# Kernel optimization log

Hardware: AMD Instinct MI355X
Metric: run time of the kernel (lower is better)

The kernel has to match this reference:

```python
import jax, jax.numpy as jnp
import numpy as np
import math

N = 50000
E = 800000
C_IN = 32
C_H = 256
C_OUT = 3
DEPTH = 3
RATIO = 0.5


def setup_inputs() -> dict:
    key = jax.random.key(0)
    ks = jax.random.split(key, 16)
    s = 0.05  # keep tanh/relu in a healthy range
    f32 = jnp.float32
    return {
        "x": jax.random.normal(ks[0], (N, C_IN), f32),
        "edge_index": jax.random.randint(ks[1], (2, E), 0, N, jnp.int32).astype(jnp.int64),
        "w0_l": jax.random.normal(ks[2], (C_IN, C_H), f32) * s,
        "w0_r": jax.random.normal(ks[3], (C_IN, C_H), f32) * s,
        "b0": jax.random.normal(ks[4], (C_H,), f32) * s,
        "dwl": jax.random.normal(ks[5], (DEPTH, C_H, C_H), f32) * s,
        "dwr": jax.random.normal(ks[6], (DEPTH, C_H, C_H), f32) * s,
        "db": jax.random.normal(ks[7], (DEPTH, C_H), f32) * s,
        "pool_w": jax.random.normal(ks[8], (DEPTH, C_H), f32),
        "uwl": jax.random.normal(ks[9], (DEPTH - 1, C_H, C_H), f32) * s,
        "uwr": jax.random.normal(ks[10], (DEPTH - 1, C_H, C_H), f32) * s,
        "ub": jax.random.normal(ks[11], (DEPTH - 1, C_H), f32) * s,
        "uwl_last": jax.random.normal(ks[12], (C_H, C_OUT), f32) * s,
        "uwr_last": jax.random.normal(ks[13], (C_H, C_OUT), f32) * s,
        "ub_last": jax.random.normal(ks[14], (C_OUT,), f32) * s,
    }


def _sage_max(x, src, dst, n, wl, wr, b):
    # SAGEConv(aggr='max'): out = lin_l(max_j x_j) + lin_r(x_i)
    # dst may contain dummy index n (masked edges); slice it off.
    msg = x[src]                                            # [E, C]
    agg = jax.ops.segment_max(msg, dst, num_segments=n + 1)[:n]
    agg = jnp.where(jnp.isfinite(agg), agg, 0.0)            # empty segments -> 0 (PyG)
    return agg @ wl + b + x @ wr


def _topk_pool(x, src, dst, w, ratio):
    # PyG TopKPooling with min_score=None: score=tanh((x.w)/||w||), keep top-k, rescale.
    n = x.shape[0]
    k = math.ceil(ratio * n)
    score = jnp.tanh((x @ w) / jnp.linalg.norm(w))          # [n]
    vals, perm = jax.lax.top_k(score, k)
    x2 = x[perm] * vals[:, None]
    # relabel edges; dropped edges -> dummy node k (fixed shape, equivalent for max-agg)
    mapping = jnp.full((n + 1,), -1, jnp.int32).at[perm].set(jnp.arange(k, dtype=jnp.int32))
    nsrc, ndst = mapping[src], mapping[dst]
    valid = (nsrc >= 0) & (ndst >= 0)
    src2 = jnp.where(valid, nsrc, 0)
    dst2 = jnp.where(valid, ndst, k)
    return x2, src2, dst2, perm, k


def reference(x, edge_index, w0_l, w0_r, b0, dwl, dwr, db, pool_w,
              uwl, uwr, ub, uwl_last, uwr_last, ub_last):
    n = x.shape[0]
    src = edge_index[0].astype(jnp.int32)
    dst = edge_index[1].astype(jnp.int32)

    x = jax.nn.relu(_sage_max(x, src, dst, n, w0_l, w0_r, b0))
    xs, srcs, dsts, ns, perms = [x], [src], [dst], [n], []

    for i in range(DEPTH):
        x, src, dst, perm, n = _topk_pool(x, src, dst, pool_w[i], RATIO)
        x = jax.nn.relu(_sage_max(x, src, dst, n, dwl[i], dwr[i], db[i]))
        if i < DEPTH - 1:
            xs.append(x); srcs.append(src); dsts.append(dst); ns.append(n)
        perms.append(perm)

    for i in range(DEPTH):
        j = DEPTH - 1 - i
        res, src, dst, n, perm = xs[j], srcs[j], dsts[j], ns[j], perms[j]
        up = jnp.zeros_like(res).at[perm].set(x)
        x = res + up                                         # sum_res=True
        if i < DEPTH - 1:
            x = jax.nn.relu(_sage_max(x, src, dst, n, uwl[i], uwr[i], ub[i]))
        else:
            x = _sage_max(x, src, dst, n, uwl_last, uwr_last, ub_last)

    return jnp.tanh(x) * 0.5
```

## Files before the change

kernel.cpp:

```cpp
#include <hip/hip_runtime.h>
#include <math.h>

#define E_NUM 800000
#define CH 256

typedef __attribute__((ext_vector_type(8))) short short8;
typedef __attribute__((ext_vector_type(4))) float float4v;

__device__ __forceinline__ unsigned f2key(float s) {
  unsigned b = __float_as_uint(s);
  return (b & 0x80000000u) ? ~b : (b | 0x80000000u);
}


__global__ __launch_bounds__(256) void k_deg(const int* __restrict__ dst, int n,
                                             int* __restrict__ deg) {
  int e = blockIdx.x * 256 + threadIdx.x;
  if (e < E_NUM) { int d = dst[e]; if (d < n) atomicAdd(&deg[d], 1); }
}

__global__ __launch_bounds__(256) void k_scan_block(const int* __restrict__ deg, int n,
                                                    int* __restrict__ incl,
                                                    int* __restrict__ bsum) {
  __shared__ int s[256];
  int i = blockIdx.x * 256 + threadIdx.x;
  int v = (i < n) ? deg[i] : 0;
  s[threadIdx.x] = v;
  __syncthreads();
  for (int o = 1; o < 256; o <<= 1) {
    int t = (threadIdx.x >= o) ? s[threadIdx.x - o] : 0;
    __syncthreads();
    s[threadIdx.x] += t;
    __syncthreads();
  }
  if (i < n) incl[i] = s[threadIdx.x];
  if (threadIdx.x == 255) bsum[blockIdx.x] = s[255];
}

__global__ void k_scan_bsum(int* bsum, int nb, int* total_out) {
  if (threadIdx.x == 0 && blockIdx.x == 0) {
    int acc = 0;
    for (int b = 0; b < nb; b++) { int v = bsum[b]; bsum[b] = acc; acc += v; }
    total_out[0] = acc;
  }
}

__global__ __launch_bounds__(256) void k_scan_final(const int* __restrict__ deg,
                                                    const int* __restrict__ incl,
                                                    const int* __restrict__ bsum, int n,
                                                    int* __restrict__ row,
                                                    int* __restrict__ cursor) {
  int i = blockIdx.x * 256 + threadIdx.x;
  if (i < n) {
    int r = incl[i] - deg[i] + bsum[blockIdx.x];
    row[i] = r;
    cursor[i] = r;
  }
}

__global__ __launch_bounds__(256) void k_fill(const int* __restrict__ src,
                                              const int* __restrict__ dst, int n,
                                              int* __restrict__ cursor,
                                              int* __restrict__ col) {
  int e = blockIdx.x * 256 + threadIdx.x;
  if (e < E_NUM) {
    int d = dst[e];
    if (d < n) { int p = atomicAdd(&cursor[d], 1); col[p] = src[e]; }
  }
}

__global__ __launch_bounds__(256) void k_relabel_deg(const int* __restrict__ srcIn,
                                                     const int* __restrict__ dstIn,
                                                     const int* __restrict__ mapping,
                                                     int kNew, int* __restrict__ srcOut,
                                                     int* __restrict__ dstOut,
                                                     int* __restrict__ deg) {
  int e = blockIdx.x * 256 + threadIdx.x;
  if (e >= E_NUM) return;
  int ns = mapping[srcIn[e]];
  int nd = mapping[dstIn[e]];
  if (ns >= 0 && nd >= 0) {
    srcOut[e] = ns;
    dstOut[e] = nd;
    atomicAdd(&deg[nd], 1);
  } else {
    srcOut[e] = 0;
    dstOut[e] = kNew;
  }
}


__device__ __forceinline__ float4 fmax4(float4 a, float4 b) {
  return make_float4(fmaxf(a.x, b.x), fmaxf(a.y, b.y), fmaxf(a.z, b.z), fmaxf(a.w, b.w));
}

__global__ __launch_bounds__(256) void k_aggmax32(const float* __restrict__ x,
                                                  const int* __restrict__ row,
                                                  const int* __restrict__ col,
                                                  float* __restrict__ out, int n) {
  int node = blockIdx.x * 8 + threadIdx.x / 32;
  int c = threadIdx.x % 32;
  if (node >= n) return;
  int e0 = row[node], e1 = row[node + 1];
  float m0 = -INFINITY, m1 = -INFINITY, m2 = -INFINITY, m3 = -INFINITY;
  int e = e0;
  for (; e + 4 <= e1; e += 4) {
    int s0 = col[e], s1 = col[e + 1], s2 = col[e + 2], s3 = col[e + 3];
    float v0 = x[(size_t)s0 * 32 + c];
    float v1 = x[(size_t)s1 * 32 + c];
    float v2 = x[(size_t)s2 * 32 + c];
    float v3 = x[(size_t)s3 * 32 + c];
    m0 = fmaxf(m0, v0); m1 = fmaxf(m1, v1); m2 = fmaxf(m2, v2); m3 = fmaxf(m3, v3);
  }
  for (; e < e1; e++) m0 = fmaxf(m0, x[(size_t)col[e] * 32 + c]);
  float m = fmaxf(fmaxf(m0, m1), fmaxf(m2, m3));
  out[(size_t)node * 32 + c] = (e1 > e0) ? m : 0.0f;
}

__global__ __launch_bounds__(256) void k_aggmax4(const float* __restrict__ x,
                                                 const int* __restrict__ row,
                                                 const int* __restrict__ col,
                                                 float* __restrict__ out, int n) {
  int lane = threadIdx.x & 63;
  int node = blockIdx.x * 4 + (threadIdx.x >> 6);
  if (node >= n) return;
  int e0 = row[node], e1 = row[node + 1];
  float4 m0 = make_float4(-INFINITY, -INFINITY, -INFINITY, -INFINITY);
  float4 m1 = m0, m2 = m0, m3 = m0;
  int e = e0;
  for (; e + 4 <= e1; e += 4) {
    int s0 = col[e], s1 = col[e + 1], s2 = col[e + 2], s3 = col[e + 3];
    float4 v0 = *(const float4*)&x[(size_t)s0 * CH + lane * 4];
    float4 v1 = *(const float4*)&x[(size_t)s1 * CH + lane * 4];
    float4 v2 = *(const float4*)&x[(size_t)s2 * CH + lane * 4];
    float4 v3 = *(const float4*)&x[(size_t)s3 * CH + lane * 4];
    m0 = fmax4(m0, v0); m1 = fmax4(m1, v1); m2 = fmax4(m2, v2); m3 = fmax4(m3, v3);
  }
  for (; e < e1; e++)
    m0 = fmax4(m0, *(const float4*)&x[(size_t)col[e] * CH + lane * 4]);
  float4 m = fmax4(fmax4(m0, m1), fmax4(m2, m3));
  if (e1 <= e0) m = make_float4(0.f, 0.f, 0.f, 0.f);
  *(float4*)&out[(size_t)node * CH + lane * 4] = m;
}

__device__ __forceinline__ float b2f(unsigned short s) {
  return __uint_as_float(((unsigned)s) << 16);
}
__device__ __forceinline__ float4 bmax4(float4 m, ushort4 v) {
  m.x = fmaxf(m.x, b2f(v.x));
  m.y = fmaxf(m.y, b2f(v.y));
  m.z = fmaxf(m.z, b2f(v.z));
  m.w = fmaxf(m.w, b2f(v.w));
  return m;
}

__global__ __launch_bounds__(256) void k_aggmax4_b16(const unsigned short* __restrict__ xb,
                                                     const int* __restrict__ row,
                                                     const int* __restrict__ col,
                                                     float* __restrict__ out, int n) {
  int lane = threadIdx.x & 63;
  int node = blockIdx.x * 4 + (threadIdx.x >> 6);
  if (node >= n) return;
  int e0 = row[node], e1 = row[node + 1];
  float4 m0 = make_float4(-INFINITY, -INFINITY, -INFINITY, -INFINITY);
  float4 m1 = m0, m2 = m0, m3 = m0;
  int e = e0;
  for (; e + 4 <= e1; e += 4) {
    int s0 = col[e], s1 = col[e + 1], s2 = col[e + 2], s3 = col[e + 3];
    ushort4 v0 = *(const ushort4*)&xb[(size_t)s0 * CH + lane * 4];
    ushort4 v1 = *(const ushort4*)&xb[(size_t)s1 * CH + lane * 4];
    ushort4 v2 = *(const ushort4*)&xb[(size_t)s2 * CH + lane * 4];
    ushort4 v3 = *(const ushort4*)&xb[(size_t)s3 * CH + lane * 4];
    m0 = bmax4(m0, v0); m1 = bmax4(m1, v1); m2 = bmax4(m2, v2); m3 = bmax4(m3, v3);
  }
  for (; e < e1; e++)
    m0 = bmax4(m0, *(const ushort4*)&xb[(size_t)col[e] * CH + lane * 4]);
  float4 m = fmax4(fmax4(m0, m1), fmax4(m2, m3));
  if (e1 <= e0) m = make_float4(0.f, 0.f, 0.f, 0.f);
  *(float4*)&out[(size_t)node * CH + lane * 4] = m;
}


__global__ __launch_bounds__(256) void k_wprep(const float* __restrict__ src,
                                               unsigned short* __restrict__ dst, int K,
                                               int nmat) {
  int idx = blockIdx.x * 256 + threadIdx.x;
  int total = nmat * K * 256;
  if (idx >= total) return;
  int n = idx % 256;
  int k = (idx / 256) % K;
  int m = idx / (256 * K);
  float v = src[idx];
  unsigned u = __float_as_uint(v);
  unsigned h = u & 0xFFFF0000u;
  float r = v - __uint_as_float(h);
  unsigned short hs = (unsigned short)(h >> 16);
  unsigned short ls = (unsigned short)(__float_as_uint(r) >> 16);
  int ib = k >> 5, kk = k & 31;
  size_t base = (size_t)m * 2 * K * 256;
  size_t o = ((size_t)ib * 256 + n) * 32 + kk;
  dst[base + o] = hs;
  dst[base + (size_t)K * 256 + o] = ls;
}


#define KSTR 40

__global__ __launch_bounds__(256) void k_gemm_mfma(
    const float* __restrict__ A1, const float* __restrict__ A2,
    const unsigned short* __restrict__ W1t, const unsigned short* __restrict__ W2t,
    const float* __restrict__ bias, float* __restrict__ out, int M, int K, int scatter,
    const int* __restrict__ perm, const float* __restrict__ scw,
    float* __restrict__ score, unsigned* __restrict__ hist1) {
  __shared__ unsigned short As_h[64 * KSTR], As_l[64 * KSTR];
  __shared__ unsigned short Bs_h[256 * KSTR], Bs_l[256 * KSTR];
  __shared__ float sred[4][64];
  const int t = threadIdx.x;
  const int wave = t >> 6, lane = t & 63;
  const int l15 = lane & 15, qd = lane >> 4;
  const int bm0 = blockIdx.x * 64;
  float4v acc[4][4];
#pragma unroll
  for (int a = 0; a < 4; a++)
#pragma unroll
    for (int b = 0; b < 4; b++) acc[a][b] = (float4v)0.f;
  const int sa_m = t >> 2;
  const int sa_kc = (t & 3) * 8;
  const int rok = (bm0 + sa_m) < M;
  const int nIb = K >> 5;
  for (int ib = 0; ib < 2 * nIb; ib++) {
    const float* A = (ib < nIb) ? A1 : A2;
    const unsigned short* Wt = (ib < nIb) ? W1t : W2t;
    int ib0 = (ib < nIb) ? ib : ib - nIb;
    float va[8];
    {
      const float* ap = &A[(size_t)(bm0 + sa_m) * K + (ib0 << 5) + sa_kc];
      float4 v0 = rok ? *(const float4*)ap : make_float4(0, 0, 0, 0);
      float4 v1 = rok ? *(const float4*)(ap + 4) : make_float4(0, 0, 0, 0);
      va[0] = v0.x; va[1] = v0.y; va[2] = v0.z; va[3] = v0.w;
      va[4] = v1.x; va[5] = v1.y; va[6] = v1.z; va[7] = v1.w;
    }
    unsigned hp[4], lp[4];
#pragma unroll
    for (int e = 0; e < 4; e++) {
      unsigned u0 = __float_as_uint(va[2 * e]);
      unsigned u1 = __float_as_uint(va[2 * e + 1]);
      unsigned h0 = u0 & 0xFFFF0000u, h1 = u1 & 0xFFFF0000u;
      float r0 = va[2 * e] - __uint_as_float(h0);
      float r1 = va[2 * e + 1] - __uint_as_float(h1);
      hp[e] = (h0 >> 16) | h1;
      lp[e] = (__float_as_uint(r0) >> 16) | (__float_as_uint(r1) & 0xFFFF0000u);
    }
    size_t ro = ((size_t)ib0 * 256 + t) * 32;
    uint4 bh0 = *(const uint4*)&Wt[ro];
    uint4 bh1 = *(const uint4*)&Wt[ro + 8];
    uint4 bh2 = *(const uint4*)&Wt[ro + 16];
    uint4 bh3 = *(const uint4*)&Wt[ro + 24];
    size_t rl = (size_t)K * 256 + ro;
    uint4 bl0 = *(const uint4*)&Wt[rl];
    uint4 bl1 = *(const uint4*)&Wt[rl + 8];
    uint4 bl2 = *(const uint4*)&Wt[rl + 16];
    uint4 bl3 = *(const uint4*)&Wt[rl + 24];
    __syncthreads();
    *(uint4*)&As_h[sa_m * KSTR + sa_kc] = make_uint4(hp[0], hp[1], hp[2], hp[3]);
    *(uint4*)&As_l[sa_m * KSTR + sa_kc] = make_uint4(lp[0], lp[1], lp[2], lp[3]);
    *(uint4*)&Bs_h[t * KSTR + 0] = bh0;
    *(uint4*)&Bs_h[t * KSTR + 8] = bh1;
    *(uint4*)&Bs_h[t * KSTR + 16] = bh2;
    *(uint4*)&Bs_h[t * KSTR + 24] = bh3;
    *(uint4*)&Bs_l[t * KSTR + 0] = bl0;
    *(uint4*)&Bs_l[t * KSTR + 8] = bl1;
    *(uint4*)&Bs_l[t * KSTR + 16] = bl2;
    *(uint4*)&Bs_l[t * KSTR + 24] = bl3;
    __syncthreads();
    short8 ah[4], al[4], bh[4], bl[4];
#pragma unroll
    for (int mt = 0; mt < 4; mt++) {
      int r = (mt * 16 + l15) * KSTR + qd * 8;
      ah[mt] = *(const short8*)&As_h[r];
      al[mt] = *(const short8*)&As_l[r];
    }
#pragma unroll
    for (int nt = 0; nt < 4; nt++) {
      int r = (wave * 64 + nt * 16 + l15) * KSTR + qd * 8;
      bh[nt] = *(const short8*)&Bs_h[r];
      bl[nt] = *(const short8*)&Bs_l[r];
    }
#pragma unroll
    for (int mt = 0; mt < 4; mt++)
#pragma unroll
      for (int nt = 0; nt < 4; nt++) {
        acc[mt][nt] =
            __builtin_amdgcn_mfma_f32_16x16x32_bf16(bh[nt], ah[mt], acc[mt][nt], 0, 0, 0);
        acc[mt][nt] =
            __builtin_amdgcn_mfma_f32_16x16x32_bf16(bl[nt], ah[mt], acc[mt][nt], 0, 0, 0);
        acc[mt][nt] =
            __builtin_amdgcn_mfma_f32_16x16x32_bf16(bh[nt], al[mt], acc[mt][nt], 0, 0, 0);
      }
  }
  const int col0 = wave * 64;
  if (scw) {
    if (t < 64) { sred[0][t] = 0.f; sred[1][t] = 0.f; sred[2][t] = 0.f; sred[3][t] = 0.f; }
    __syncthreads();
  }
  float bias4[4][4], scw4[4][4];
#pragma unroll
  for (int nt = 0; nt < 4; nt++) {
    int cb = col0 + nt * 16 + qd * 4;
    *(float4*)bias4[nt] = *(const float4*)&bias[cb];
    if (scw) *(float4*)scw4[nt] = *(const float4*)&scw[cb];
  }
#pragma unroll
  for (int mt = 0; mt < 4; mt++) {
    int p = bm0 + mt * 16 + l15;
    float sp = 0.f;
    if (p < M) {
      if (scatter) {
        size_t rb = (size_t)perm[p] * CH + col0 + qd * 4;
#pragma unroll
        for (int nt = 0; nt < 4; nt++) {
          float* dp = &out[rb + nt * 16];
          float4 old = *(const float4*)dp;
          float4 v;
          v.x = old.x + fmaxf(acc[mt][nt][0] + bias4[nt][0], 0.f);
          v.y = old.y + fmaxf(acc[mt][nt][1] + bias4[nt][1], 0.f);
          v.z = old.z + fmaxf(acc[mt][nt][2] + bias4[nt][2], 0.f);
          v.w = old.w + fmaxf(acc[mt][nt][3] + bias4[nt][3], 0.f);
          *(float4*)dp = v;
        }
      } else {
        size_t rb = (size_t)p * CH + col0 + qd * 4;
#pragma unroll
        for (int nt = 0; nt < 4; nt++) {
          float4 v;
          v.x = fmaxf(acc[mt][nt][0] + bias4[nt][0], 0.f);
          v.y = fmaxf(acc[mt][nt][1] + bias4[nt][1], 0.f);
          v.z = fmaxf(acc[mt][nt][2] + bias4[nt][2], 0.f);
          v.w = fmaxf(acc[mt][nt][3] + bias4[nt][3], 0.f);
          *(float4*)&out[rb + nt * 16] = v;
          if (scw)
            sp += v.x * scw4[nt][0] + v.y * scw4[nt][1] + v.z * scw4[nt][2] +
                  v.w * scw4[nt][3];
        }
      }
    }
    if (scw) {
      sp += __shfl_xor(sp, 16);
      sp += __shfl_xor(sp, 32);
      if (qd == 0) sred[wave][mt * 16 + l15] = sp;
    }
  }
  if (scw) {
    __syncthreads();
    if (t < 64 && bm0 + t < M) {
      float s = sred[0][t] + sred[1][t] + sred[2][t] + sred[3][t];
      score[bm0 + t] = s;
      atomicAdd(&hist1[f2key(s) >> 16], 1u);
    }
  }
}


__global__ __launch_bounds__(1024) void k_resolve(const unsigned* __restrict__ hist,
                                                  unsigned* __restrict__ state, int pass,
                                                  int k0) {
  __shared__ unsigned csum[1024];
  int t = threadIdx.x;
  int base = 65535 - 64 * t;
  unsigned s = 0;
  for (int j = 0; j < 64; j++) s += hist[base - j];
  csum[t] = s;
  __syncthreads();
  for (int o = 1; o < 1024; o <<= 1) {
    unsigned v = (t >= o) ? csum[t - o] : 0u;
    __syncthreads();
    csum[t] += v;
    __syncthreads();
  }
  unsigned cumBefore = csum[t] - s;
  unsigned kneed = (pass == 0) ? (unsigned)k0 : state[5];
  if (cumBefore < kneed && kneed <= cumBefore + s) {
    unsigned cum = cumBefore;
    for (int j = 0; j < 64; j++) {
      unsigned c = hist[base - j];
      if (cum + c >= kneed) {
        unsigned bucket = (unsigned)(base - j);
        if (pass == 0) {
          state[4] = bucket;
          state[5] = kneed - cum;
        } else {
          state[0] = (state[4] << 16) | bucket;
          state[1] = kneed - cum;
          state[2] = 0u;
          state[3] = 0u;
        }
        break;
      }
      cum += c;
    }
  }
}

__global__ __launch_bounds__(256) void k_hist2(const float* __restrict__ score, int n,
                                               const unsigned* __restrict__ state,
                                               unsigned* __restrict__ hist2) {
  int i = blockIdx.x * 256 + threadIdx.x;
  if (i >= n) return;
  unsigned u = f2key(score[i]);
  if ((u >> 16) == state[4]) atomicAdd(&hist2[u & 0xFFFFu], 1u);
}

__global__ __launch_bounds__(256) void k_compact(const float* __restrict__ score, int n,
                                                 unsigned* __restrict__ state,
                                                 int* __restrict__ perm,
                                                 int* __restrict__ mapping) {
  int i = blockIdx.x * 256 + threadIdx.x;
  if (i > n) return;
  if (i == n) { mapping[n] = -1; return; }
  unsigned Kth = state[0];
  unsigned kneed = state[1];
  unsigned u = f2key(score[i]);
  int m = -1;
  if (u > Kth) {
    unsigned p = atomicAdd(&state[2], 1u);
    perm[p] = i;
    m = (int)p;
  } else if (u == Kth) {
    unsigned tt = atomicAdd(&state[3], 1u);
    if (tt < kneed) {
      unsigned p = atomicAdd(&state[2], 1u);
      perm[p] = i;
      m = (int)p;
    }
  }
  mapping[i] = m;
}

__global__ __launch_bounds__(256) void k_gather(const float* __restrict__ x,
                                                const int* __restrict__ perm,
                                                const float* __restrict__ score,
                                                const float* __restrict__ pw,
                                                float* __restrict__ out, int k) {
  int lane = threadIdx.x & 63;
  int node = blockIdx.x * 4 + (threadIdx.x >> 6);
  float4 w4 = *(const float4*)&pw[lane * 4];
  float nn = w4.x * w4.x + w4.y * w4.y + w4.z * w4.z + w4.w * w4.w;
#pragma unroll
  for (int o = 32; o > 0; o >>= 1) nn += __shfl_down(nn, o);
  nn = __shfl(nn, 0);
  if (node >= k) return;
  int i = perm[node];
  float tv = tanhf(score[i] / sqrtf(nn));
  float4 v = *(const float4*)&x[(size_t)i * CH + lane * 4];
  v.x *= tv; v.y *= tv; v.z *= tv; v.w *= tv;
  *(float4*)&out[(size_t)node * CH + lane * 4] = v;
}


__device__ __forceinline__ unsigned short f2b_rn(float f) {
  unsigned u = __float_as_uint(f);
  u += 0x7FFFu + ((u >> 16) & 1u);
  return (unsigned short)(u >> 16);
}

__global__ __launch_bounds__(256) void k_cvtb16(const float* __restrict__ x,
                                                unsigned short* __restrict__ xb, int n) {
  int lane = threadIdx.x & 63;
  int node = blockIdx.x * 4 + (threadIdx.x >> 6);
  if (node >= n) return;
  float4 a = *(const float4*)&x[(size_t)node * CH + lane * 4];
  ushort4 o;
  o.x = f2b_rn(a.x); o.y = f2b_rn(a.y); o.z = f2b_rn(a.z); o.w = f2b_rn(a.w);
  *(ushort4*)&xb[(size_t)node * CH + lane * 4] = o;
}

__global__ __launch_bounds__(256) void k_final(const unsigned short* __restrict__ XB,
                                               const int* __restrict__ row,
                                               const int* __restrict__ col,
                                               const float* __restrict__ wl,
                                               const float* __restrict__ wr,
                                               const float* __restrict__ b,
                                               float* __restrict__ out, int n) {
  int lane = threadIdx.x & 63;
  int node = blockIdx.x * 4 + (threadIdx.x >> 6);
  if (node >= n) return;
  int e0 = row[node], e1 = row[node + 1];
  float4 m0 = make_float4(-INFINITY, -INFINITY, -INFINITY, -INFINITY);
  float4 m1 = m0, m2 = m0, m3 = m0;
  int e = e0;
  for (; e + 4 <= e1; e += 4) {
    int s0 = col[e], s1 = col[e + 1], s2 = col[e + 2], s3 = col[e + 3];
    ushort4 v0 = *(const ushort4*)&XB[(size_t)s0 * CH + lane * 4];
    ushort4 v1 = *(const ushort4*)&XB[(size_t)s1 * CH + lane * 4];
    ushort4 v2 = *(const ushort4*)&XB[(size_t)s2 * CH + lane * 4];
    ushort4 v3 = *(const ushort4*)&XB[(size_t)s3 * CH + lane * 4];
    m0 = bmax4(m0, v0); m1 = bmax4(m1, v1); m2 = bmax4(m2, v2); m3 = bmax4(m3, v3);
  }
  for (; e < e1; e++)
    m0 = bmax4(m0, *(const ushort4*)&XB[(size_t)col[e] * CH + lane * 4]);
  float4 m = fmax4(fmax4(m0, m1), fmax4(m2, m3));
  if (e1 <= e0) m = make_float4(0.f, 0.f, 0.f, 0.f);
  ushort4 sv4 = *(const ushort4*)&XB[(size_t)node * CH + lane * 4];
  float wlv[12], wrv[12];
  *(float4*)&wlv[0] = ((const float4*)(wl + 12 * lane))[0];
  *(float4*)&wlv[4] = ((const float4*)(wl + 12 * lane))[1];
  *(float4*)&wlv[8] = ((const float4*)(wl + 12 * lane))[2];
  *(float4*)&wrv[0] = ((const float4*)(wr + 12 * lane))[0];
  *(float4*)&wrv[4] = ((const float4*)(wr + 12 * lane))[1];
  *(float4*)&wrv[8] = ((const float4*)(wr + 12 * lane))[2];
  float av[4] = {m.x, m.y, m.z, m.w};
  float sv[4] = {b2f(sv4.x), b2f(sv4.y), b2f(sv4.z), b2f(sv4.w)};
  float p[3] = {0.f, 0.f, 0.f};
#pragma unroll
  for (int q = 0; q < 4; q++)
#pragma unroll
    for (int jj = 0; jj < 3; jj++)
      p[jj] += av[q] * wlv[q * 3 + jj] + sv[q] * wrv[q * 3 + jj];
#pragma unroll
  for (int jj = 0; jj < 3; jj++) {
#pragma unroll
    for (int o = 32; o > 0; o >>= 1) p[jj] += __shfl_down(p[jj], o);
  }
  if (lane == 0) {
#pragma unroll
    for (int jj = 0; jj < 3; jj++)
      out[(size_t)node * 3 + jj] = tanhf(p[jj] + b[jj]) * 0.5f;
  }
}


extern "C" void kernel_launch(void* const* d_in, const int* in_sizes, int n_in,
                              void* d_out, int out_size, void* d_ws, size_t ws_size,
                              hipStream_t stream) {
  (void)in_sizes; (void)n_in; (void)out_size; (void)ws_size;
  const float* xin = (const float*)d_in[0];
  const int* ei = (const int*)d_in[1];
  const int* src0 = ei;
  const int* dst0 = ei + E_NUM;
  const float* w0l = (const float*)d_in[2];
  const float* w0r = (const float*)d_in[3];
  const float* b0 = (const float*)d_in[4];
  const float* dwl = (const float*)d_in[5];
  const float* dwr = (const float*)d_in[6];
  const float* db = (const float*)d_in[7];
  const float* poolw = (const float*)d_in[8];
  const float* uwl = (const float*)d_in[9];
  const float* uwr = (const float*)d_in[10];
  const float* ub = (const float*)d_in[11];
  const float* uwlL = (const float*)d_in[12];
  const float* uwrL = (const float*)d_in[13];
  const float* ubL = (const float*)d_in[14];
  float* out = (float*)d_out;

  char* base = (char*)d_ws;
  size_t off = 0;
  auto alloc = [&](size_t bytes) -> void* {
    void* p = base + off;
    off = (off + bytes + 255) & ~(size_t)255;
    return p;
  };

  const int n0 = 50000, n1 = 25000, n2 = 12500, n3 = 6250;
  float* X0 = (float*)alloc((size_t)n0 * CH * 4);
  float* X1 = (float*)alloc((size_t)n1 * CH * 4);
  float* X2 = (float*)alloc((size_t)n2 * CH * 4);
  float* AGG = (float*)alloc((size_t)n1 * CH * 4);
  float* PD = (float*)alloc((size_t)n1 * CH * 4);
  unsigned short* XB = (unsigned short*)alloc((size_t)n0 * CH * 2);
  unsigned short* X1B = (unsigned short*)alloc((size_t)n1 * CH * 2);
  unsigned short* X2B = (unsigned short*)alloc((size_t)n2 * CH * 2);
  int* eA = (int*)alloc((size_t)2 * E_NUM * 4);
  int* eB = (int*)alloc((size_t)2 * E_NUM * 4);
  int* col0 = (int*)alloc((size_t)E_NUM * 4);
  int* col1 = (int*)alloc((size_t)E_NUM * 4);
  int* col2 = (int*)alloc((size_t)E_NUM * 4);
  int* col3 = (int*)alloc((size_t)E_NUM * 4);
  int* row0 = (int*)alloc((size_t)(n0 + 1) * 4);
  int* row1 = (int*)alloc((size_t)(n1 + 1) * 4);
  int* row2 = (int*)alloc((size_t)(n2 + 1) * 4);
  int* row3 = (int*)alloc((size_t)(n3 + 1) * 4);
  int* map1 = (int*)alloc((size_t)(n0 + 1) * 4);
  int* map2 = (int*)alloc((size_t)(n1 + 1) * 4);
  int* map3 = (int*)alloc((size_t)(n2 + 1) * 4);
  int* perm1 = (int*)alloc((size_t)n1 * 4);
  int* perm2 = (int*)alloc((size_t)n2 * 4);
  int* perm3 = (int*)alloc((size_t)n3 * 4);
  float* score = (float*)alloc((size_t)n0 * 4);
  int* deg = (int*)alloc((size_t)n0 * 4);
  int* incl = (int*)alloc((size_t)n0 * 4);
  int* cursor = (int*)alloc((size_t)n0 * 4);
  int* bsum = (int*)alloc((size_t)256 * 4);
  unsigned* state = (unsigned*)alloc(1024);
  unsigned* hist = (unsigned*)alloc((size_t)2 * 65536 * 4);
  const size_t WSZ = (size_t)2 * 256 * 256;
  unsigned short* Wt0l = (unsigned short*)alloc((size_t)2 * 32 * 256 * 2);
  unsigned short* Wt0r = (unsigned short*)alloc((size_t)2 * 32 * 256 * 2);
  unsigned short* Wtdl = (unsigned short*)alloc(3 * WSZ * 2);
  unsigned short* Wtdr = (unsigned short*)alloc(3 * WSZ * 2);
  unsigned short* Wtul = (unsigned short*)alloc(2 * WSZ * 2);
  unsigned short* Wtur = (unsigned short*)alloc(2 * WSZ * 2);

  const int EG = (E_NUM + 255) / 256;

  k_wprep<<<(32 * 256 + 255) / 256, 256, 0, stream>>>(w0l, Wt0l, 32, 1);
  k_wprep<<<(32 * 256 + 255) / 256, 256, 0, stream>>>(w0r, Wt0r, 32, 1);
  k_wprep<<<(3 * 256 * 256 + 255) / 256, 256, 0, stream>>>(dwl, Wtdl, 256, 3);
  k_wprep<<<(3 * 256 * 256 + 255) / 256, 256, 0, stream>>>(dwr, Wtdr, 256, 3);
  k_wprep<<<(2 * 256 * 256 + 255) / 256, 256, 0, stream>>>(uwl, Wtul, 256, 2);
  k_wprep<<<(2 * 256 * 256 + 255) / 256, 256, 0, stream>>>(uwr, Wtur, 256, 2);

  auto csrRest = [&](const int* esrc, const int* edst, int n, int* rowp, int* colp) {
    int nb = (n + 255) / 256;
    k_scan_block<<<nb, 256, 0, stream>>>(deg, n, incl, bsum);
    k_scan_bsum<<<1, 1, 0, stream>>>(bsum, nb, rowp + n);
    k_scan_final<<<nb, 256, 0, stream>>>(deg, incl, bsum, n, rowp, cursor);
    k_fill<<<EG, 256, 0, stream>>>(esrc, edst, n, cursor, colp);
  };

  auto poolLevel = [&](const float* X, const float* pw, int n, int k, int* mapping,
                       int* permL, const int* esrcIn, const int* edstIn, int* esrcOut,
                       int* edstOut, float* Pout) {
    k_resolve<<<1, 1024, 0, stream>>>(hist, state, 0, k);
    k_hist2<<<(n + 255) / 256, 256, 0, stream>>>(score, n, state, hist + 65536);
    k_resolve<<<1, 1024, 0, stream>>>(hist + 65536, state, 1, k);
    k_compact<<<(n + 1 + 255) / 256, 256, 0, stream>>>(score, n, state, permL, mapping);
    k_gather<<<(k + 3) / 4, 256, 0, stream>>>(X, permL, score, pw, Pout, k);
    hipMemsetAsync(deg, 0, (size_t)k * 4, stream);
    k_relabel_deg<<<EG, 256, 0, stream>>>(esrcIn, edstIn, mapping, k, esrcOut, edstOut,
                                          deg);
  };

  auto gemm = [&](const float* A1, const float* A2, const unsigned short* W1t,
                  const unsigned short* W2t, const float* bias, float* o, int M, int K,
                  int scatter, const int* prm, const float* scw, float* sc) {
    if (scw) hipMemsetAsync(hist, 0, (size_t)2 * 65536 * 4, stream);
    k_gemm_mfma<<<(M + 63) / 64, 256, 0, stream>>>(A1, A2, W1t, W2t, bias, o, M, K,
                                                   scatter, prm, scw, sc, hist);
  };

  hipMemsetAsync(deg, 0, (size_t)n0 * 4, stream);
  k_deg<<<EG, 256, 0, stream>>>(dst0, n0, deg);
  csrRest(src0, dst0, n0, row0, col0);
  k_aggmax32<<<(n0 + 7) / 8, 256, 0, stream>>>(xin, row0, col0, AGG, n0);
  gemm(AGG, xin, Wt0l, Wt0r, b0, X0, n0, 32, 0, nullptr, poolw + 0 * CH, score);

  poolLevel(X0, poolw + 0 * CH, n0, n1, map1, perm1, src0, dst0, eA, eA + E_NUM, PD);
  csrRest(eA, eA + E_NUM, n1, row1, col1);
  k_aggmax4<<<(n1 + 3) / 4, 256, 0, stream>>>(PD, row1, col1, AGG, n1);
  gemm(AGG, PD, Wtdl + 0 * WSZ, Wtdr + 0 * WSZ, db + 0 * CH, X1, n1, 256, 0, nullptr,
       poolw + 1 * CH, score);

  poolLevel(X1, poolw + 1 * CH, n1, n2, map2, perm2, eA, eA + E_NUM, eB, eB + E_NUM, PD);
  csrRest(eB, eB + E_NUM, n2, row2, col2);
  k_aggmax4<<<(n2 + 3) / 4, 256, 0, stream>>>(PD, row2, col2, AGG, n2);
  gemm(AGG, PD, Wtdl + 1 * WSZ, Wtdr + 1 * WSZ, db + 1 * CH, X2, n2, 256, 0, nullptr,
       poolw + 2 * CH, score);

  poolLevel(X2, poolw + 2 * CH, n2, n3, map3, perm3, eB, eB + E_NUM, eA, eA + E_NUM, PD);
  csrRest(eA, eA + E_NUM, n3, row3, col3);
  k_aggmax4<<<(n3 + 3) / 4, 256, 0, stream>>>(PD, row3, col3, AGG, n3);
  gemm(AGG, PD, Wtdl + 2 * WSZ, Wtdr + 2 * WSZ, db + 2 * CH, X2, n3, 256, 1, perm3,
       nullptr, nullptr);

  k_cvtb16<<<(n2 + 3) / 4, 256, 0, stream>>>(X2, X2B, n2);
  k_aggmax4_b16<<<(n2 + 3) / 4, 256, 0, stream>>>(X2B, row2, col2, AGG, n2);
  gemm(AGG, X2, Wtul + 0 * WSZ, Wtur + 0 * WSZ, ub + 0 * CH, X1, n2, 256, 1, perm2,
       nullptr, nullptr);

  k_cvtb16<<<(n1 + 3) / 4, 256, 0, stream>>>(X1, X1B, n1);
  k_aggmax4_b16<<<(n1 + 3) / 4, 256, 0, stream>>>(X1B, row1, col1, AGG, n1);
  gemm(AGG, X1, Wtul + 1 * WSZ, Wtur + 1 * WSZ, ub + 1 * CH, X0, n1, 256, 1, perm1,
       nullptr, nullptr);

  k_cvtb16<<<(n0 + 3) / 4, 256, 0, stream>>>(X0, XB, n0);
  k_final<<<(n0 + 3) / 4, 256, 0, stream>>>(XB, row0, col0, uwlL, uwrL, ubL, out, n0);
}
```

Before: 864.9 us.

## Use packed u16 max for bf16 aggregation and load GEMM B directly to registers

Max aggregation over bf16 features now compares raw bits with packed unsigned 16-bit max, relying on the features being non-negative after relu, and drops the float conversion per element. The GEMM kernel no longer stages weight tiles through shared memory; each wave loads its MFMA B fragments straight from global memory. This cuts ALU work and LDS traffic, at the cost of assuming non-negative inputs and issuing more uncoalesced global weight loads.

```diff
diff --git a/kernel.cpp b/kernel.cpp
--- a/kernel.cpp
+++ b/kernel.cpp
@@ -10,6 +10,12 @@
 __device__ __forceinline__ unsigned f2key(float s) {
   unsigned b = __float_as_uint(s);
   return (b & 0x80000000u) ? ~b : (b | 0x80000000u);
+}
+
+__device__ __forceinline__ unsigned pkmax_u16(unsigned a, unsigned b) {
+  unsigned d;
+  asm("v_pk_max_u16 %0, %1, %2" : "=v"(d) : "v"(a), "v"(b));
+  return d;
 }
 
 
@@ -146,13 +152,6 @@
 __device__ __forceinline__ float b2f(unsigned short s) {
   return __uint_as_float(((unsigned)s) << 16);
 }
-__device__ __forceinline__ float4 bmax4(float4 m, ushort4 v) {
-  m.x = fmaxf(m.x, b2f(v.x));
-  m.y = fmaxf(m.y, b2f(v.y));
-  m.z = fmaxf(m.z, b2f(v.z));
-  m.w = fmaxf(m.w, b2f(v.w));
-  return m;
-}
 
 __global__ __launch_bounds__(256) void k_aggmax4_b16(const unsigned short* __restrict__ xb,
                                                      const int* __restrict__ row,
@@ -162,21 +161,31 @@
   int node = blockIdx.x * 4 + (threadIdx.x >> 6);
   if (node >= n) return;
   int e0 = row[node], e1 = row[node + 1];
-  float4 m0 = make_float4(-INFINITY, -INFINITY, -INFINITY, -INFINITY);
-  float4 m1 = m0, m2 = m0, m3 = m0;
+  uint2 m0 = make_uint2(0u, 0u), m1 = m0, m2 = m0, m3 = m0;
   int e = e0;
   for (; e + 4 <= e1; e += 4) {
     int s0 = col[e], s1 = col[e + 1], s2 = col[e + 2], s3 = col[e + 3];
-    ushort4 v0 = *(const ushort4*)&xb[(size_t)s0 * CH + lane * 4];
-    ushort4 v1 = *(const ushort4*)&xb[(size_t)s1 * CH + lane * 4];
-    ushort4 v2 = *(const ushort4*)&xb[(size_t)s2 * CH + lane * 4];
-    ushort4 v3 = *(const ushort4*)&xb[(size_t)s3 * CH + lane * 4];
-    m0 = bmax4(m0, v0); m1 = bmax4(m1, v1); m2 = bmax4(m2, v2); m3 = bmax4(m3, v3);
-  }
-  for (; e < e1; e++)
-    m0 = bmax4(m0, *(const ushort4*)&xb[(size_t)col[e] * CH + lane * 4]);
-  float4 m = fmax4(fmax4(m0, m1), fmax4(m2, m3));
-  if (e1 <= e0) m = make_float4(0.f, 0.f, 0.f, 0.f);
+    uint2 v0 = *(const uint2*)&xb[(size_t)s0 * CH + lane * 4];
+    uint2 v1 = *(const uint2*)&xb[(size_t)s1 * CH + lane * 4];
+    uint2 v2 = *(const uint2*)&xb[(size_t)s2 * CH + lane * 4];
+    uint2 v3 = *(const uint2*)&xb[(size_t)s3 * CH + lane * 4];
+    m0.x = pkmax_u16(m0.x, v0.x); m0.y = pkmax_u16(m0.y, v0.y);
+    m1.x = pkmax_u16(m1.x, v1.x); m1.y = pkmax_u16(m1.y, v1.y);
+    m2.x = pkmax_u16(m2.x, v2.x); m2.y = pkmax_u16(m2.y, v2.y);
+    m3.x = pkmax_u16(m3.x, v3.x); m3.y = pkmax_u16(m3.y, v3.y);
+  }
+  for (; e < e1; e++) {
+    uint2 v = *(const uint2*)&xb[(size_t)col[e] * CH + lane * 4];
+    m0.x = pkmax_u16(m0.x, v.x);
+    m0.y = pkmax_u16(m0.y, v.y);
+  }
+  m0.x = pkmax_u16(pkmax_u16(m0.x, m1.x), pkmax_u16(m2.x, m3.x));
+  m0.y = pkmax_u16(pkmax_u16(m0.y, m1.y), pkmax_u16(m2.y, m3.y));
+  float4 m;
+  m.x = b2f((unsigned short)(m0.x & 0xFFFFu));
+  m.y = b2f((unsigned short)(m0.x >> 16));
+  m.z = b2f((unsigned short)(m0.y & 0xFFFFu));
+  m.w = b2f((unsigned short)(m0.y >> 16));
   *(float4*)&out[(size_t)node * CH + lane * 4] = m;
 }
 
@@ -213,7 +222,6 @@
     const int* __restrict__ perm, const float* __restrict__ scw,
     float* __restrict__ score, unsigned* __restrict__ hist1) {
   __shared__ unsigned short As_h[64 * KSTR], As_l[64 * KSTR];
-  __shared__ unsigned short Bs_h[256 * KSTR], Bs_l[256 * KSTR];
   __shared__ float sred[4][64];
   const int t = threadIdx.x;
   const int wave = t >> 6, lane = t & 63;
@@ -240,6 +248,13 @@
       va[0] = v0.x; va[1] = v0.y; va[2] = v0.z; va[3] = v0.w;
       va[4] = v1.x; va[5] = v1.y; va[6] = v1.z; va[7] = v1.w;
     }
+    short8 bh[4], bl[4];
+#pragma unroll
+    for (int nt = 0; nt < 4; nt++) {
+      size_t rowb = ((size_t)ib0 * 256 + wave * 64 + nt * 16 + l15) * 32 + qd * 8;
+      bh[nt] = *(const short8*)&Wt[rowb];
+      bl[nt] = *(const short8*)&Wt[(size_t)K * 256 + rowb];
+    }
     unsigned hp[4], lp[4];
 #pragma unroll
     for (int e = 0; e < 4; e++) {
@@ -251,40 +266,16 @@
       hp[e] = (h0 >> 16) | h1;
       lp[e] = (__float_as_uint(r0) >> 16) | (__float_as_uint(r1) & 0xFFFF0000u);
     }
-    size_t ro = ((size_t)ib0 * 256 + t) * 32;
-    uint4 bh0 = *(const uint4*)&Wt[ro];
-    uint4 bh1 = *(const uint4*)&Wt[ro + 8];
-    uint4 bh2 = *(const uint4*)&Wt[ro + 16];
-    uint4 bh3 = *(const uint4*)&Wt[ro + 24];
-    size_t rl = (size_t)K * 256 + ro;
-    uint4 bl0 = *(const uint4*)&Wt[rl];
-    uint4 bl1 = *(const uint4*)&Wt[rl + 8];
-    uint4 bl2 = *(const uint4*)&Wt[rl + 16];
-    uint4 bl3 = *(const uint4*)&Wt[rl + 24];
     __syncthreads();
     *(uint4*)&As_h[sa_m * KSTR + sa_kc] = make_uint4(hp[0], hp[1], hp[2], hp[3]);
     *(uint4*)&As_l[sa_m * KSTR + sa_kc] = make_uint4(lp[0], lp[1], lp[2], lp[3]);
-    *(uint4*)&Bs_h[t * KSTR + 0] = bh0;
-    *(uint4*)&Bs_h[t * KSTR + 8] = bh1;
-    *(uint4*)&Bs_h[t * KSTR + 16] = bh2;
-    *(uint4*)&Bs_h[t * KSTR + 24] = bh3;
-    *(uint4*)&Bs_l[t * KSTR + 0] = bl0;
-    *(uint4*)&Bs_l[t * KSTR + 8] = bl1;
-    *(uint4*)&Bs_l[t * KSTR + 16] = bl2;
-    *(uint4*)&Bs_l[t * KSTR + 24] = bl3;
-    __syncthreads();
-    short8 ah[4], al[4], bh[4], bl[4];
+    __syncthreads();
+    short8 ah[4], al[4];
 #pragma unroll
     for (int mt = 0; mt < 4; mt++) {
       int r = (mt * 16 + l15) * KSTR + qd * 8;
       ah[mt] = *(const short8*)&As_h[r];
       al[mt] = *(const short8*)&As_l[r];
-    }
-#pragma unroll
-    for (int nt = 0; nt < 4; nt++) {
-      int r = (wave * 64 + nt * 16 + l15) * KSTR + qd * 8;
-      bh[nt] = *(const short8*)&Bs_h[r];
-      bl[nt] = *(const short8*)&Bs_l[r];
     }
 #pragma unroll
     for (int mt = 0; mt < 4; mt++)
@@ -485,21 +476,31 @@
   int node = blockIdx.x * 4 + (threadIdx.x >> 6);
   if (node >= n) return;
   int e0 = row[node], e1 = row[node + 1];
-  float4 m0 = make_float4(-INFINITY, -INFINITY, -INFINITY, -INFINITY);
-  float4 m1 = m0, m2 = m0, m3 = m0;
+  uint2 m0 = make_uint2(0u, 0u), m1 = m0, m2 = m0, m3 = m0;
   int e = e0;
   for (; e + 4 <= e1; e += 4) {
     int s0 = col[e], s1 = col[e + 1], s2 = col[e + 2], s3 = col[e + 3];
-    ushort4 v0 = *(const ushort4*)&XB[(size_t)s0 * CH + lane * 4];
-    ushort4 v1 = *(const ushort4*)&XB[(size_t)s1 * CH + lane * 4];
-    ushort4 v2 = *(const ushort4*)&XB[(size_t)s2 * CH + lane * 4];
-    ushort4 v3 = *(const ushort4*)&XB[(size_t)s3 * CH + lane * 4];
-    m0 = bmax4(m0, v0); m1 = bmax4(m1, v1); m2 = bmax4(m2, v2); m3 = bmax4(m3, v3);
-  }
-  for (; e < e1; e++)
-    m0 = bmax4(m0, *(const ushort4*)&XB[(size_t)col[e] * CH + lane * 4]);
-  float4 m = fmax4(fmax4(m0, m1), fmax4(m2, m3));
-  if (e1 <= e0) m = make_float4(0.f, 0.f, 0.f, 0.f);
+    uint2 v0 = *(const uint2*)&XB[(size_t)s0 * CH + lane * 4];
+    uint2 v1 = *(const uint2*)&XB[(size_t)s1 * CH + lane * 4];
+    uint2 v2 = *(const uint2*)&XB[(size_t)s2 * CH + lane * 4];
+    uint2 v3 = *(const uint2*)&XB[(size_t)s3 * CH + lane * 4];
+    m0.x = pkmax_u16(m0.x, v0.x); m0.y = pkmax_u16(m0.y, v0.y);
+    m1.x = pkmax_u16(m1.x, v1.x); m1.y = pkmax_u16(m1.y, v1.y);
+    m2.x = pkmax_u16(m2.x, v2.x); m2.y = pkmax_u16(m2.y, v2.y);
+    m3.x = pkmax_u16(m3.x, v3.x); m3.y = pkmax_u16(m3.y, v3.y);
+  }
+  for (; e < e1; e++) {
+    uint2 v = *(const uint2*)&XB[(size_t)col[e] * CH + lane * 4];
+    m0.x = pkmax_u16(m0.x, v.x);
+    m0.y = pkmax_u16(m0.y, v.y);
+  }
+  m0.x = pkmax_u16(pkmax_u16(m0.x, m1.x), pkmax_u16(m2.x, m3.x));
+  m0.y = pkmax_u16(pkmax_u16(m0.y, m1.y), pkmax_u16(m2.y, m3.y));
+  float av[4];
+  av[0] = b2f((unsigned short)(m0.x & 0xFFFFu));
+  av[1] = b2f((unsigned short)(m0.x >> 16));
+  av[2] = b2f((unsigned short)(m0.y & 0xFFFFu));
+  av[3] = b2f((unsigned short)(m0.y >> 16));
   ushort4 sv4 = *(const ushort4*)&XB[(size_t)node * CH + lane * 4];
   float wlv[12], wrv[12];
   *(float4*)&wlv[0] = ((const float4*)(wl + 12 * lane))[0];
@@ -508,7 +509,6 @@
   *(float4*)&wrv[0] = ((const float4*)(wr + 12 * lane))[0];
   *(float4*)&wrv[4] = ((const float4*)(wr + 12 * lane))[1];
   *(float4*)&wrv[8] = ((const float4*)(wr + 12 * lane))[2];
-  float av[4] = {m.x, m.y, m.z, m.w};
   float sv[4] = {b2f(sv4.x), b2f(sv4.y), b2f(sv4.z), b2f(sv4.w)};
   float p[3] = {0.f, 0.f, 0.f};
 #pragma unroll
```

Result: faster. 847.5 us (-2.0%).
